# Kernel optimization log

Measured on AMD Instinct MI355X. Metric: run time of the kernel, lower is better.

The kernel has to match this reference:

```python
import jax, jax.numpy as jnp
import numpy as np
import math

EMBED_DIM = 768
NUM_HEADS = 12
N_QUBITS = 96
D_K = N_QUBITS // NUM_HEADS


def setup_inputs() -> dict:
    key = jax.random.key(0)
    k1, k2, k3 = jax.random.split(key, 3)
    x = jax.random.normal(k1, (8, 1024, EMBED_DIM), dtype=jnp.float32)
    # trainable RY angles, one per qubit (tq.RY has_params init ~ uniform small)
    theta = jax.random.uniform(k2, (N_QUBITS,), dtype=jnp.float32, minval=-math.pi, maxval=math.pi)
    # combine_heads: nn.Linear(n_qubits, embed_dim, bias=False) -> weight [out, in]
    W_combine = jax.random.normal(k3, (EMBED_DIM, N_QUBITS), dtype=jnp.float32) / math.sqrt(N_QUBITS)
    return {"x": x, "theta": theta, "W_combine": W_combine}


def reference(x, theta, W_combine):
    B, S, _ = x.shape
    # Quantum circuit is unentangled: per wire i, RX(x_i) then RY(theta_i) on |0>,
    # <PauliZ> = cos(x_i) * cos(theta_i). Fully batched over (B, S).
    xs = x[..., :N_QUBITS]                      # [B, S, nq]
    q_vecs = jnp.cos(xs) * jnp.cos(theta)       # [B, S, nq]

    # split heads: [B, H, S, d_k]; q == k == v
    q = q_vecs.reshape(B, S, NUM_HEADS, D_K).transpose(0, 2, 1, 3)

    scores = jnp.einsum('bhsd,bhtd->bhst', q, q) / math.sqrt(D_K)  # [B,H,S,S]
    probs = jax.nn.softmax(scores, axis=-1)
    attn = jnp.einsum('bhst,bhtd->bhsd', probs, q)                 # [B,H,S,d_k]
    attn = attn.transpose(0, 2, 1, 3).reshape(B, S, N_QUBITS)
    return attn @ W_combine.T                                       # [B,S,embed_dim]
```

## Files before the change

### kernel.cpp

```cpp
#include <hip/hip_runtime.h>
#include <hip/hip_bf16.h>

#define SEQ 1024
#define DK 8
#define NH 12
#define BATCH 8
#define NQ 96
#define ED 768

typedef __attribute__((ext_vector_type(8))) _Float16 half8;
typedef __attribute__((ext_vector_type(2))) __fp16 fp16x2;
typedef __attribute__((ext_vector_type(4))) float floatx4;
typedef __attribute__((ext_vector_type(2))) unsigned uint2v;

__device__ __forceinline__ float fast_exp2(float x) {
#if __has_builtin(__builtin_amdgcn_exp2f)
    return __builtin_amdgcn_exp2f(x);
#else
    return exp2f(x);
#endif
}

__device__ __forceinline__ unsigned pkh(float lo, float hi) {
    union { fp16x2 h; unsigned u; } v;
    v.h = __builtin_amdgcn_cvt_pkrtz(lo, hi);
    return v.u;
}

__global__ __launch_bounds__(512) void attn_kernel(
    const float* __restrict__ x, const float* __restrict__ theta,
    _Float16* __restrict__ attn )
{
    __shared__ __align__(16) _Float16 qv[SEQ * DK];
    __shared__ __align__(16) _Float16 qvt[32 * 512];
    __shared__ __align__(16) _Float16 pt[8 * 576];

    const int chunk = blockIdx.x;
    const int h     = blockIdx.y;
    const int b     = blockIdx.z;
    const int tid   = threadIdx.x;

    const float SQS = 0.71419170f;

    float ct[8];
    #pragma unroll
    for (int k = 0; k < 8; ++k) ct[k] = __cosf(theta[h * DK + k]);

    #pragma unroll
    for (int it = 0; it < 2; ++it) {
        const int s = tid + it * 512;
        const float* xp = x + ((size_t)(b * SEQ + s)) * ED + h * DK;
        const float4 v0 = *(const float4*)xp;
        const float4 v1 = *(const float4*)(xp + 4);
        float q[8];
        q[0] = __cosf(v0.x) * ct[0]; q[1] = __cosf(v0.y) * ct[1];
        q[2] = __cosf(v0.z) * ct[2]; q[3] = __cosf(v0.w) * ct[3];
        q[4] = __cosf(v1.x) * ct[4]; q[5] = __cosf(v1.y) * ct[5];
        q[6] = __cosf(v1.z) * ct[6]; q[7] = __cosf(v1.w) * ct[7];
        union { half8 v; _Float16 e[8]; } row;
        #pragma unroll
        for (int k = 0; k < 8; ++k) row.e[k] = (_Float16)(q[k] * SQS);
        *(half8*)&qv[s * DK] = row.v;
        const int e0 = (s >> 5) * 512 + ((s >> 3) & 3) * 128 + (s & 7);
        #pragma unroll
        for (int k = 0; k < 8; ++k) qvt[e0 + k * 8] = (_Float16)q[k];
    }
    {
        const int ww = tid >> 4, qq = (tid >> 2) & 3, np = tid & 3;
        const int n0 = 8 + np * 2;
        const int e  = ww * 512 + qq * 128 + n0 * 8;
        #pragma unroll
        for (int j = 0; j < 8; ++j) { qvt[e + j] = (_Float16)0.0f; qvt[e + 8 + j] = (_Float16)0.0f; }
    }
    __syncthreads();

    const int w    = tid >> 6;
    const int lane = tid & 63;
    const int l15  = lane & 15;
    const int qt   = lane >> 4;
    const int m0w  = chunk * 128 + w * 16;

    _Float16* zp = &qvt[72];
    _Float16* myp = &pt[w * 576];

    const half8 bfm = *(const half8*)((qt == 0) ? &qv[(m0w + l15) * DK] : zp);

    const _Float16* pa0 = (qt == 0) ? &qv[l15 * DK]        : zp;
    const _Float16* pa1 = (qt == 0) ? &qv[(16 + l15) * DK] : zp;
    const int ainc = (qt == 0) ? 32 * DK : 0;
    const _Float16* pv = &qvt[qt * 128 + l15 * 8];

    _Float16* pw0 = &myp[l15 * 36 + qt * 4];
    _Float16* pw1 = pw0 + 16;
    const _Float16* pr = &myp[l15 * 36 + qt * 8];

    floatx4 acc = {0.f, 0.f, 0.f, 0.f};
    float lacc = 0.f;
    const floatx4 zc = {0.f, 0.f, 0.f, 0.f};

    {
        const half8 af0 = *(const half8*)pa0;  pa0 += ainc;
        const half8 af1 = *(const half8*)pa1;  pa1 += ainc;
        floatx4 d0 = __builtin_amdgcn_mfma_f32_16x16x32_f16(af0, bfm, zc, 0, 0, 0);
        floatx4 d1 = __builtin_amdgcn_mfma_f32_16x16x32_f16(af1, bfm, zc, 0, 0, 0);
        const float e00 = fast_exp2(d0[0]), e01 = fast_exp2(d0[1]);
        const float e02 = fast_exp2(d0[2]), e03 = fast_exp2(d0[3]);
        const float e10 = fast_exp2(d1[0]), e11 = fast_exp2(d1[1]);
        const float e12 = fast_exp2(d1[2]), e13 = fast_exp2(d1[3]);
        lacc += ((e00 + e01) + (e02 + e03)) + ((e10 + e11) + (e12 + e13));
        *(uint2v*)pw0 = (uint2v){pkh(e00, e01), pkh(e02, e03)};
        *(uint2v*)pw1 = (uint2v){pkh(e10, e11), pkh(e12, e13)};
    }

    #pragma unroll 2
    for (int win = 1; win < 32; ++win) {
        const half8 paf = *(const half8*)pr;
        const half8 vf  = *(const half8*)pv;   pv += 512;

        const half8 af0 = *(const half8*)pa0;  pa0 += ainc;
        const half8 af1 = *(const half8*)pa1;  pa1 += ainc;
        floatx4 d0 = __builtin_amdgcn_mfma_f32_16x16x32_f16(af0, bfm, zc, 0, 0, 0);
        floatx4 d1 = __builtin_amdgcn_mfma_f32_16x16x32_f16(af1, bfm, zc, 0, 0, 0);

        const float e00 = fast_exp2(d0[0]), e01 = fast_exp2(d0[1]);
        const float e02 = fast_exp2(d0[2]), e03 = fast_exp2(d0[3]);
        const float e10 = fast_exp2(d1[0]), e11 = fast_exp2(d1[1]);
        const float e12 = fast_exp2(d1[2]), e13 = fast_exp2(d1[3]);
        lacc += ((e00 + e01) + (e02 + e03)) + ((e10 + e11) + (e12 + e13));

        *(uint2v*)pw0 = (uint2v){pkh(e00, e01), pkh(e02, e03)};
        *(uint2v*)pw1 = (uint2v){pkh(e10, e11), pkh(e12, e13)};

        acc = __builtin_amdgcn_mfma_f32_16x16x32_f16(paf, vf, acc, 0, 0, 0);
    }

    {
        const half8 paf = *(const half8*)pr;
        const half8 vf  = *(const half8*)pv;
        acc = __builtin_amdgcn_mfma_f32_16x16x32_f16(paf, vf, acc, 0, 0, 0);
    }

    lacc += __shfl_xor(lacc, 16);
    lacc += __shfl_xor(lacc, 32);

    #pragma unroll
    for (int r = 0; r < 4; ++r) {
        const float lsum = __shfl(lacc, qt * 4 + r);
        const float val  = acc[r] * __builtin_amdgcn_rcpf(lsum);
        if (l15 < 8) {
            const int m = m0w + qt * 4 + r;
            attn[((size_t)(b * SEQ + m)) * NQ + h * DK + l15] = (_Float16)val;
        }
    }
}

__global__ __launch_bounds__(256) void wconv_kernel(
    const float* __restrict__ W, _Float16* __restrict__ Wh)
{
    const int i = blockIdx.x * 256 + threadIdx.x;
    const float4 v = ((const float4*)W)[i];
    union { unsigned u[2]; double d; } o;
    o.u[0] = pkh(v.x, v.y);
    o.u[1] = pkh(v.z, v.w);
    ((double*)Wh)[i] = o.d;
}

__global__ __launch_bounds__(256) void proj_kernel(
    const _Float16* __restrict__ attn, const _Float16* __restrict__ Wh,
    float* __restrict__ out)
{
    const int tid  = threadIdx.x;
    const int w    = tid >> 6;
    const int lane = tid & 63;
    const int l15  = lane & 15;
    const int quad = lane >> 4;

    const int m0 = blockIdx.y * 64 + w * 16;
    const int n0 = blockIdx.x * 64;

    const size_t abase = ((size_t)(m0 + l15)) * NQ + quad * 8;
    half8 af0 = *(const half8*)(attn + abase);
    half8 af1 = *(const half8*)(attn + abase + 32);
    half8 af2 = *(const half8*)(attn + abase + 64);

    floatx4 acc[4];
    #pragma unroll
    for (int c = 0; c < 4; ++c) acc[c] = (floatx4){0.f, 0.f, 0.f, 0.f};

    #pragma unroll
    for (int c = 0; c < 4; ++c) {
        const size_t bbase = ((size_t)(n0 + c * 16 + l15)) * NQ + quad * 8;
        half8 b0 = *(const half8*)(Wh + bbase);
        half8 b1 = *(const half8*)(Wh + bbase + 32);
        half8 b2 = *(const half8*)(Wh + bbase + 64);
        acc[c] = __builtin_amdgcn_mfma_f32_16x16x32_f16(af0, b0, acc[c], 0, 0, 0);
        acc[c] = __builtin_amdgcn_mfma_f32_16x16x32_f16(af1, b1, acc[c], 0, 0, 0);
        acc[c] = __builtin_amdgcn_mfma_f32_16x16x32_f16(af2, b2, acc[c], 0, 0, 0);
    }

    #pragma unroll
    for (int c = 0; c < 4; ++c)
        #pragma unroll
        for (int r = 0; r < 4; ++r)
            out[((size_t)(m0 + quad * 4 + r)) * ED + n0 + c * 16 + l15] = acc[c][r];
}

extern "C" void kernel_launch(void* const* d_in, const int* in_sizes, int n_in,
                              void* d_out, int out_size, void* d_ws, size_t ws_size,
                              hipStream_t stream) {
    const float* x     = (const float*)d_in[0];
    const float* theta = (const float*)d_in[1];
    const float* W     = (const float*)d_in[2];
    float* out = (float*)d_out;

    _Float16* attn = (_Float16*)d_ws;
    _Float16* Wh   = (_Float16*)((char*)d_ws + (size_t)BATCH * SEQ * NQ * 2);

    wconv_kernel<<<dim3(ED * NQ / 4 / 256), 256, 0, stream>>>(W, Wh);
    attn_kernel<<<dim3(8, NH, BATCH), 512, 0, stream>>>(x, theta, attn);
    proj_kernel<<<dim3(ED / 64, (BATCH * SEQ) / 64), 256, 0, stream>>>(attn, Wh, out);
}
```

Baseline: 120.4 us.

## Transpose P in registers with permlane swaps and fold row-sum into MFMA

Replaces the LDS round trip for the probability tile (write P, then read it back as an MFMA A operand) with v_permlane32/16_swap register shuffles. The V operand gains a column of ones, so the softmax denominator comes out of the PV MFMA itself and the scalar lacc accumulation and its cross-lane reductions go away. LDS usage shrinks and launch bounds now request 6 waves/EU occupancy. The exchange is extra permlane instructions, and the row sums are now accumulated in the MFMA from fp16-rounded exponentials rather than in fp32.

```diff
diff --git a/kernel.cpp b/kernel.cpp
--- a/kernel.cpp
+++ b/kernel.cpp
@@ -11,7 +11,6 @@
 typedef __attribute__((ext_vector_type(8))) _Float16 half8;
 typedef __attribute__((ext_vector_type(2))) __fp16 fp16x2;
 typedef __attribute__((ext_vector_type(4))) float floatx4;
-typedef __attribute__((ext_vector_type(2))) unsigned uint2v;
 
 __device__ __forceinline__ float fast_exp2(float x) {
 #if __has_builtin(__builtin_amdgcn_exp2f)
@@ -27,13 +26,31 @@
     return v.u;
 }
 
-__global__ __launch_bounds__(512) void attn_kernel(
+__device__ __forceinline__ void pl32_swap(unsigned &a, unsigned &b) {
+#if __has_builtin(__builtin_amdgcn_permlane32_swap)
+    auto r = __builtin_amdgcn_permlane32_swap(a, b, false, false);
+    a = r[0]; b = r[1];
+#else
+    asm("v_permlane32_swap_b32 %0, %1" : "+v"(a), "+v"(b));
+#endif
+}
+__device__ __forceinline__ void pl16_swap(unsigned &a, unsigned &b) {
+#if __has_builtin(__builtin_amdgcn_permlane16_swap)
+    auto r = __builtin_amdgcn_permlane16_swap(a, b, false, false);
+    a = r[0]; b = r[1];
+#else
+    asm("v_permlane16_swap_b32 %0, %1" : "+v"(a), "+v"(b));
+#endif
+}
+
+__global__ __launch_bounds__(512, 6) void attn_kernel(
     const float* __restrict__ x, const float* __restrict__ theta,
     _Float16* __restrict__ attn )
 {
     __shared__ __align__(16) _Float16 qv[SEQ * DK];
-    __shared__ __align__(16) _Float16 qvt[32 * 512];
-    __shared__ __align__(16) _Float16 pt[8 * 576];
+    __shared__ __align__(16) _Float16 qvt2[32 * 256];
+    __shared__ __align__(16) _Float16 zbuf[16];
+    __shared__ __align__(16) _Float16 obuf[8];
 
     const int chunk = blockIdx.x;
     const int h     = blockIdx.y;
@@ -45,6 +62,9 @@
     float ct[8];
     #pragma unroll
     for (int k = 0; k < 8; ++k) ct[k] = __cosf(theta[h * DK + k]);
+
+    if (tid < 16) zbuf[tid] = (_Float16)0.0f;
+    if (tid >= 16 && tid < 24) obuf[tid - 16] = (_Float16)1.0f;
 
     #pragma unroll
     for (int it = 0; it < 2; ++it) {
@@ -61,16 +81,9 @@
         #pragma unroll
         for (int k = 0; k < 8; ++k) row.e[k] = (_Float16)(q[k] * SQS);
         *(half8*)&qv[s * DK] = row.v;
-        const int e0 = (s >> 5) * 512 + ((s >> 3) & 3) * 128 + (s & 7);
+        const int e0 = (s >> 5) * 256 + ((s >> 3) & 3) * 64 + (s & 7);
         #pragma unroll
-        for (int k = 0; k < 8; ++k) qvt[e0 + k * 8] = (_Float16)q[k];
-    }
-    {
-        const int ww = tid >> 4, qq = (tid >> 2) & 3, np = tid & 3;
-        const int n0 = 8 + np * 2;
-        const int e  = ww * 512 + qq * 128 + n0 * 8;
-        #pragma unroll
-        for (int j = 0; j < 8; ++j) { qvt[e + j] = (_Float16)0.0f; qvt[e + 8 + j] = (_Float16)0.0f; }
+        for (int k = 0; k < 8; ++k) qvt2[e0 + k * 8] = (_Float16)q[k];
     }
     __syncthreads();
 
@@ -80,72 +93,50 @@
     const int qt   = lane >> 4;
     const int m0w  = chunk * 128 + w * 16;
 
-    _Float16* zp = &qvt[72];
-    _Float16* myp = &pt[w * 576];
-
-    const half8 bfm = *(const half8*)((qt == 0) ? &qv[(m0w + l15) * DK] : zp);
-
-    const _Float16* pa0 = (qt == 0) ? &qv[l15 * DK]        : zp;
-    const _Float16* pa1 = (qt == 0) ? &qv[(16 + l15) * DK] : zp;
+    const half8 bfm = *(const half8*)((qt == 0) ? &qv[(m0w + l15) * DK] : zbuf);
+
+    const _Float16* pa0 = (qt == 0) ? &qv[l15 * DK]        : zbuf;
+    const _Float16* pa1 = (qt == 0) ? &qv[(16 + l15) * DK] : zbuf;
     const int ainc = (qt == 0) ? 32 * DK : 0;
-    const _Float16* pv = &qvt[qt * 128 + l15 * 8];
-
-    _Float16* pw0 = &myp[l15 * 36 + qt * 4];
-    _Float16* pw1 = pw0 + 16;
-    const _Float16* pr = &myp[l15 * 36 + qt * 8];
+
+    const _Float16* pv;
+    int pvinc;
+    if (l15 < 8)       { pv = &qvt2[qt * 64 + l15 * 8]; pvinc = 256; }
+    else if (l15 == 8) { pv = obuf;                     pvinc = 0;   }
+    else               { pv = zbuf;                     pvinc = 0;   }
 
     floatx4 acc = {0.f, 0.f, 0.f, 0.f};
-    float lacc = 0.f;
     const floatx4 zc = {0.f, 0.f, 0.f, 0.f};
 
-    {
+    #pragma unroll 2
+    for (int win = 0; win < 32; ++win) {
         const half8 af0 = *(const half8*)pa0;  pa0 += ainc;
         const half8 af1 = *(const half8*)pa1;  pa1 += ainc;
+        const half8 vf  = *(const half8*)pv;   pv += pvinc;
+
         floatx4 d0 = __builtin_amdgcn_mfma_f32_16x16x32_f16(af0, bfm, zc, 0, 0, 0);
         floatx4 d1 = __builtin_amdgcn_mfma_f32_16x16x32_f16(af1, bfm, zc, 0, 0, 0);
+
         const float e00 = fast_exp2(d0[0]), e01 = fast_exp2(d0[1]);
         const float e02 = fast_exp2(d0[2]), e03 = fast_exp2(d0[3]);
         const float e10 = fast_exp2(d1[0]), e11 = fast_exp2(d1[1]);
         const float e12 = fast_exp2(d1[2]), e13 = fast_exp2(d1[3]);
-        lacc += ((e00 + e01) + (e02 + e03)) + ((e10 + e11) + (e12 + e13));
-        *(uint2v*)pw0 = (uint2v){pkh(e00, e01), pkh(e02, e03)};
-        *(uint2v*)pw1 = (uint2v){pkh(e10, e11), pkh(e12, e13)};
-    }
-
-    #pragma unroll 2
-    for (int win = 1; win < 32; ++win) {
-        const half8 paf = *(const half8*)pr;
-        const half8 vf  = *(const half8*)pv;   pv += 512;
-
-        const half8 af0 = *(const half8*)pa0;  pa0 += ainc;
-        const half8 af1 = *(const half8*)pa1;  pa1 += ainc;
-        floatx4 d0 = __builtin_amdgcn_mfma_f32_16x16x32_f16(af0, bfm, zc, 0, 0, 0);
-        floatx4 d1 = __builtin_amdgcn_mfma_f32_16x16x32_f16(af1, bfm, zc, 0, 0, 0);
-
-        const float e00 = fast_exp2(d0[0]), e01 = fast_exp2(d0[1]);
-        const float e02 = fast_exp2(d0[2]), e03 = fast_exp2(d0[3]);
-        const float e10 = fast_exp2(d1[0]), e11 = fast_exp2(d1[1]);
-        const float e12 = fast_exp2(d1[2]), e13 = fast_exp2(d1[3]);
-        lacc += ((e00 + e01) + (e02 + e03)) + ((e10 + e11) + (e12 + e13));
-
-        *(uint2v*)pw0 = (uint2v){pkh(e00, e01), pkh(e02, e03)};
-        *(uint2v*)pw1 = (uint2v){pkh(e10, e11), pkh(e12, e13)};
-
-        acc = __builtin_amdgcn_mfma_f32_16x16x32_f16(paf, vf, acc, 0, 0, 0);
-    }
-
-    {
-        const half8 paf = *(const half8*)pr;
-        const half8 vf  = *(const half8*)pv;
-        acc = __builtin_amdgcn_mfma_f32_16x16x32_f16(paf, vf, acc, 0, 0, 0);
-    }
-
-    lacc += __shfl_xor(lacc, 16);
-    lacc += __shfl_xor(lacc, 32);
+
+        unsigned c0 = pkh(e00, e01), c1 = pkh(e02, e03);
+        unsigned c2 = pkh(e10, e11), c3 = pkh(e12, e13);
+        pl32_swap(c0, c2);
+        pl32_swap(c1, c3);
+        pl16_swap(c0, c2);
+        pl16_swap(c1, c3);
+        union { half8 h; unsigned u[4]; } pa;
+        pa.u[0] = c0; pa.u[1] = c1; pa.u[2] = c2; pa.u[3] = c3;
+
+        acc = __builtin_amdgcn_mfma_f32_16x16x32_f16(pa.h, vf, acc, 0, 0, 0);
+    }
 
     #pragma unroll
     for (int r = 0; r < 4; ++r) {
-        const float lsum = __shfl(lacc, qt * 4 + r);
+        const float lsum = __shfl(acc[r], (lane & 48) + 8);
         const float val  = acc[r] * __builtin_amdgcn_rcpf(lsum);
         if (l15 < 8) {
             const int m = m0w + qt * 4 + r;
```

New measurement: 103.4 us, median of 2. -14.1%, faster.
